# Optimization experiments

Hardware: AMD Instinct MI355X
Metric: run time of the kernel (lower is better)

## Reference

```python
import jax, jax.numpy as jnp
import numpy as np

E = 65536
MUL0, MUL1 = 32, 16              # multiplicities of 0e and 1o in irreps_in1/out
FC_IN, FC_HID = 64, 64
WNUMEL = MUL0*MUL0 + MUL1*MUL0 + MUL0*MUL1 + MUL1*MUL1  # 2304
SILU_NORM = 1.6790                # e3nn normalize2mom constant for silu
ISQRT3 = float(1.0 / np.sqrt(3.0))  # w3j entries for l<=1 paths


def setup_inputs() -> dict:
    key = jax.random.key(0)
    k1, k2, k3, k4, k5 = jax.random.split(key, 5)
    return {
        "fea_in1": jax.random.normal(k1, (E, MUL0 + 3 * MUL1), jnp.float32),
        "fea_in2": jax.random.normal(k2, (E, 4), jnp.float32),
        "fea_weight": jax.random.normal(k3, (E, FC_IN), jnp.float32),
        "W1": jax.random.normal(k4, (FC_IN, FC_HID), jnp.float32),
        "W2": jax.random.normal(k5, (FC_HID, WNUMEL), jnp.float32),
    }


def reference(fea_in1, fea_in2, fea_weight, W1, W2):
    # --- e3nn FullyConnectedNet: variance-preserving linear + normalized silu ---
    h = SILU_NORM * jax.nn.silu(fea_weight @ (W1 / np.sqrt(FC_IN)))   # [E, FC_HID]
    w = h @ (W2 / np.sqrt(FC_HID))                                    # [E, WNUMEL]

    # --- split generated per-edge weights into the 4 uvw paths ---
    s0 = MUL0 * MUL0
    s1 = s0 + MUL1 * MUL0
    s2 = s1 + MUL0 * MUL1
    w00 = w[:, :s0].reshape(E, MUL0, MUL0)     # 0e x 0e -> 0e
    w110 = w[:, s0:s1].reshape(E, MUL1, MUL0)  # 1o x 1o -> 0e
    w011 = w[:, s1:s2].reshape(E, MUL0, MUL1)  # 0e x 1o -> 1o
    w101 = w[:, s2:].reshape(E, MUL1, MUL1)    # 1o x 0e -> 1o

    # --- split irrep blocks ---
    x1_0 = fea_in1[:, :MUL0]                       # [E, 32]
    x1_1 = fea_in1[:, MUL0:].reshape(E, MUL1, 3)   # [E, 16, 3]
    x2_0 = fea_in2[:, 0]                           # [E]
    x2_1 = fea_in2[:, 1:4]                         # [E, 3]

    # path weights: sqrt(ir_out.dim / (mul_in1*mul_in2 * n_paths_to_output))
    pw00 = float(np.sqrt(1.0 / (MUL0 * 2)))
    pw110 = float(np.sqrt(1.0 / (MUL1 * 2)))
    pw011 = float(np.sqrt(3.0 / (MUL0 * 2)))
    pw101 = float(np.sqrt(3.0 / (MUL1 * 2)))

    # CG contractions (w3j(0,0,0)=1, w3j(1,1,0)=delta/sqrt3, w3j(0,1,1)=w3j(1,0,1)=delta/sqrt3)
    out0 = pw00 * jnp.einsum('eu,e,euw->ew', x1_0, x2_0, w00) \
         + (pw110 * ISQRT3) * jnp.einsum('eui,ei,euw->ew', x1_1, x2_1, w110)   # [E, 32]
    out1 = (pw011 * ISQRT3) * jnp.einsum('eu,ek,euw->ewk', x1_0, x2_1, w011) \
         + (pw101 * ISQRT3) * jnp.einsum('eui,e,euw->ewi', x1_1, x2_0, w101)   # [E, 16, 3]

    return jnp.concatenate([out0, out1.reshape(E, 3 * MUL1)], axis=1)          # [E, 80]
```

## Files before the change

### kernel.cpp

```cpp
#include <hip/hip_runtime.h>
#include <hip/hip_bf16.h>

typedef __attribute__((ext_vector_type(8)))  __bf16 bf16x8;
typedef __attribute__((ext_vector_type(16))) float  f32x16;

#define N_TILES   72
#define W2F_ELEMS (72*4*64*8)
#define W1F_ELEMS (2*4*64*8)

__device__ __forceinline__ void gload_lds16(const void* g, void* l) {
    __builtin_amdgcn_global_load_lds(
        (const __attribute__((address_space(1))) unsigned int*)g,
        (__attribute__((address_space(3))) unsigned int*)l, 16, 0, 0);
}

__device__ __forceinline__ unsigned pk_bf16(float a, float b) {
    unsigned r;
    asm("v_cvt_pk_bf16_f32 %0, %1, %2" : "=v"(r) : "v"(a), "v"(b));
    return r;
}

__global__ __launch_bounds__(256) void equiconv_prep(const float* __restrict__ W1,
                                                     const float* __restrict__ W2,
                                                     __bf16* __restrict__ W1F,
                                                     __bf16* __restrict__ W2F) {
    int idx = blockIdx.x * 256 + threadIdx.x;
    if (idx < W2F_ELEMS) {
        int j  = idx & 7;
        int ln = (idx >> 3) & 63;
        int ks = (idx >> 9) & 3;
        int t  = idx >> 11;
        int m  = 32 * t + (ln & 31);
        int c  = ks * 16 + 8 * (ln >> 5) + j;
        W2F[idx] = (__bf16)(W2[c * 2304 + m] * 0.125f);
    } else {
        int i2 = idx - W2F_ELEMS;
        if (i2 < W1F_ELEMS) {
            int j  = i2 & 7;
            int ln = (i2 >> 3) & 63;
            int ks = (i2 >> 9) & 3;
            int mt = i2 >> 11;
            int c  = 32 * mt + (ln & 31);
            int in = ks * 16 + 8 * (ln >> 5) + j;
            W1F[i2] = (__bf16)(W1[in * 64 + c] * 0.125f);
        }
    }
}

#define X10f(u, el)    smemf[(u)*129 + (el)]
#define CB1f(u, el)    smemf[4128 + (u)*129 + (el)]
#define X11f(k, u, el) smemf[6192 + ((u)*3 + (k))*129 + (el)]
#define F2f(el, j)     smemf[12384 + (el)*4 + (j)]
#define ASTG_BASE 12896

__global__ __launch_bounds__(256) void equiconv_main(const float* __restrict__ fea_in1,
                                                     const float* __restrict__ fea_in2,
                                                     const float* __restrict__ fea_w,
                                                     const __bf16* __restrict__ W2F,
                                                     const __bf16* __restrict__ W1F,
                                                     float* __restrict__ out) {
    __shared__ __align__(16) float smemf[14944];

    const int tid  = threadIdx.x;
    const int lane = tid & 63;
    const int wv   = tid >> 6;
    const int l31  = lane & 31;
    const int hi   = lane >> 5;
    const int eBlk = blockIdx.x * 128;
    const int eLoc = wv * 32 + l31;

    for (int i = tid; i < 128 * 80; i += 256) {
        float v = fea_in1[(size_t)eBlk * 80 + i];
        int el = i / 80;
        int j  = i - el * 80;
        if (j < 32) {
            X10f(j, el) = v;
        } else {
            int jj = j - 32;
            int u  = jj / 3;
            int k  = jj - u * 3;
            X11f(k, u, el) = v;
        }
    }
    for (int i = tid; i < 128 * 4; i += 256)
        F2f(i >> 2, i & 3) = fea_in2[(size_t)eBlk * 4 + i];
    __syncthreads();

    const float c110 = 0.10206207261596577f;
    for (int i = tid; i < 16 * 128; i += 256) {
        int u = i >> 7, el = i & 127;
        CB1f(u, el) = c110 * (X11f(0, u, el) * F2f(el, 1) +
                              X11f(1, u, el) * F2f(el, 2) +
                              X11f(2, u, el) * F2f(el, 3));
    }

    const f32x16 Z16 = {0,0,0,0,0,0,0,0,0,0,0,0,0,0,0,0};
    bf16x8 hfr0, hfr1, hfr2, hfr3;
    {
        bf16x8 bw[4];
        const float* pw = fea_w + (size_t)(eBlk + eLoc) * 64 + hi * 8;
#pragma unroll
        for (int ks = 0; ks < 4; ++ks) {
            float4 u0 = *(const float4*)(pw + ks * 16);
            float4 u1 = *(const float4*)(pw + ks * 16 + 4);
            bf16x8 b;
            b[0] = (__bf16)u0.x; b[1] = (__bf16)u0.y; b[2] = (__bf16)u0.z; b[3] = (__bf16)u0.w;
            b[4] = (__bf16)u1.x; b[5] = (__bf16)u1.y; b[6] = (__bf16)u1.z; b[7] = (__bf16)u1.w;
            bw[ks] = b;
        }
        f32x16 h0 = Z16, h1 = Z16;
#pragma unroll
        for (int ks = 0; ks < 4; ++ks) {
            bf16x8 a0 = *(const bf16x8*)(W1F + (size_t)((0 * 4 + ks) * 64 + lane) * 8);
            h0 = __builtin_amdgcn_mfma_f32_32x32x16_bf16(a0, bw[ks], h0, 0, 0, 0);
            bf16x8 a1 = *(const bf16x8*)(W1F + (size_t)((1 * 4 + ks) * 64 + lane) * 8);
            h1 = __builtin_amdgcn_mfma_f32_32x32x16_bf16(a1, bw[ks], h1, 0, 0, 0);
        }
        float sv[32];
#pragma unroll
        for (int r = 0; r < 16; ++r) {
            float x0 = h0[r];
            sv[r]      = 1.679f * x0 / (1.f + __expf(-x0));
            float x1 = h1[r];
            sv[16 + r] = 1.679f * x1 / (1.f + __expf(-x1));
        }
        uint4 fr[4];
#pragma unroll
        for (int ks = 0; ks < 4; ++ks) {
            const int vb = 8 * ks;
            float oa = hi ? sv[vb + 4] : sv[vb + 0];
            float ob = hi ? sv[vb + 5] : sv[vb + 1];
            float oc = hi ? sv[vb + 6] : sv[vb + 2];
            float od = hi ? sv[vb + 7] : sv[vb + 3];
            float sa = hi ? sv[vb + 0] : sv[vb + 4];
            float sb = hi ? sv[vb + 1] : sv[vb + 5];
            float sc = hi ? sv[vb + 2] : sv[vb + 6];
            float sd = hi ? sv[vb + 3] : sv[vb + 7];
            unsigned o0 = pk_bf16(oa, ob), o1 = pk_bf16(oc, od);
            unsigned s0 = pk_bf16(sa, sb), s1 = pk_bf16(sc, sd);
            unsigned r0 = (unsigned)__shfl_xor((int)s0, 32, 64);
            unsigned r1 = (unsigned)__shfl_xor((int)s1, 32, 64);
            fr[ks].x = hi ? r0 : o0;
            fr[ks].y = hi ? r1 : o1;
            fr[ks].z = hi ? o0 : r0;
            fr[ks].w = hi ? o1 : r1;
        }
        hfr0 = *(bf16x8*)&fr[0];
        hfr1 = *(bf16x8*)&fr[1];
        hfr2 = *(bf16x8*)&fr[2];
        hfr3 = *(bf16x8*)&fr[3];
    }

    const float x20  = F2f(eLoc, 0);
    const float x21a = F2f(eLoc, 1), x21b = F2f(eLoc, 2), x21c = F2f(eLoc, 3);
    const float sA0  = 0.125f * x20;
    const float s101 = 0.17677669529663687f * x20;

    float acc0[16];
    float t011[8];
    float t101[3][8];
#pragma unroll
    for (int r = 0; r < 16; ++r) acc0[r] = 0.f;
#pragma unroll
    for (int s = 0; s < 8; ++s) { t011[s] = 0.f; t101[0][s] = 0.f; t101[1][s] = 0.f; t101[2][s] = 0.f; }

    const __bf16* ASTG = (const __bf16*)(smemf + ASTG_BASE);
    char* stgb = (char*)(smemf + ASTG_BASE);
    const char* w2b = (const char*)W2F;

#define STAGE(T, BUF) {                                                           \
        const char* _s = w2b + ((size_t)(T) << 12) + wv * 1024 + (lane << 4);     \
        char* _d = stgb + ((BUF) << 12) + wv * 1024;                              \
        gload_lds16(_s, _d); }

#define EPI_W00(TT) { float cf = sA0 * X10f((TT), eLoc);                          \
        _Pragma("unroll") for (int r = 0; r < 16; ++r) acc0[r] += cf * Cv[r]; }
#define EPI_W110(TT) { float cf = CB1f((TT) - 32, eLoc);                          \
        _Pragma("unroll") for (int r = 0; r < 16; ++r) acc0[r] += cf * Cv[r]; }
#define EPI_W011(TT) { int uu = 2 * ((TT) - 48);                                  \
        float cf0 = X10f(uu, eLoc), cf1 = X10f(uu + 1, eLoc);                     \
        _Pragma("unroll") for (int r = 0; r < 16; ++r)                            \
            t011[r & 7] += (r >= 8 ? cf1 : cf0) * Cv[r]; }
#define EPI_W101(TT) { int uu = 2 * ((TT) - 64);                                  \
        float d00 = X11f(0, uu, eLoc), d01 = X11f(1, uu, eLoc), d02 = X11f(2, uu, eLoc);          \
        float d10 = X11f(0, uu + 1, eLoc), d11 = X11f(1, uu + 1, eLoc), d12 = X11f(2, uu + 1, eLoc); \
        _Pragma("unroll") for (int r = 0; r < 16; ++r) { int s = r & 7;           \
            t101[0][s] += (r >= 8 ? d10 : d00) * Cv[r];                           \
            t101[1][s] += (r >= 8 ? d11 : d01) * Cv[r];                           \
            t101[2][s] += (r >= 8 ? d12 : d02) * Cv[r]; } }

#define TILE_STEP(T, EPI) {                                                       \
        if ((T) + 1 < N_TILES) STAGE((T) + 1, bufx ^ 1);                          \
        const __bf16* tb = ASTG + (bufx << 11) + (lane << 3);                     \
        bf16x8 a0 = *(const bf16x8*)(tb);                                         \
        bf16x8 a1 = *(const bf16x8*)(tb + 512);                                   \
        bf16x8 a2 = *(const bf16x8*)(tb + 1024);                                  \
        bf16x8 a3 = *(const bf16x8*)(tb + 1536);                                  \
        f32x16 Cv;                                                                \
        Cv = __builtin_amdgcn_mfma_f32_32x32x16_bf16(a0, hfr0, Z16, 0, 0, 0);     \
        Cv = __builtin_amdgcn_mfma_f32_32x32x16_bf16(a1, hfr1, Cv, 0, 0, 0);      \
        Cv = __builtin_amdgcn_mfma_f32_32x32x16_bf16(a2, hfr2, Cv, 0, 0, 0);      \
        Cv = __builtin_amdgcn_mfma_f32_32x32x16_bf16(a3, hfr3, Cv, 0, 0, 0);      \
        EPI(T);                                                                   \
        __syncthreads();                                                          \
        bufx ^= 1; }

    int bufx = 0;
    STAGE(0, 0);
    __syncthreads();

#pragma unroll 2
    for (int t = 0; t < 32; ++t) TILE_STEP(t, EPI_W00)
#pragma unroll 2
    for (int t = 32; t < 48; ++t) TILE_STEP(t, EPI_W110)
#pragma unroll 2
    for (int t = 48; t < 64; ++t) TILE_STEP(t, EPI_W011)
#pragma unroll 2
    for (int t = 64; t < 72; ++t) TILE_STEP(t, EPI_W101)

    float* OST = smemf;
#pragma unroll
    for (int r = 0; r < 16; ++r) {
        int rv = (r & 3) + 8 * (r >> 2) + 4 * hi;
        OST[eLoc * 81 + rv] = acc0[r];
    }
#pragma unroll
    for (int s = 0; s < 8; ++s) {
        int w = (s & 3) + 8 * (s >> 2) + 4 * hi;
        float b011 = 0.125f * t011[s];
        OST[eLoc * 81 + 32 + w * 3 + 0] = x21a * b011 + s101 * t101[0][s];
        OST[eLoc * 81 + 32 + w * 3 + 1] = x21b * b011 + s101 * t101[1][s];
        OST[eLoc * 81 + 32 + w * 3 + 2] = x21c * b011 + s101 * t101[2][s];
    }
    __syncthreads();
    {
        float* og = out + (size_t)blockIdx.x * 10240;
        for (int i = tid; i < 10240; i += 256) {
            int el = i / 80;
            int j  = i - el * 80;
            og[i] = OST[el * 81 + j];
        }
    }
}

extern "C" void kernel_launch(void* const* d_in, const int* in_sizes, int n_in,
                              void* d_out, int out_size, void* d_ws, size_t ws_size,
                              hipStream_t stream) {
    const float* fea_in1 = (const float*)d_in[0];
    const float* fea_in2 = (const float*)d_in[1];
    const float* fea_w   = (const float*)d_in[2];
    const float* W1      = (const float*)d_in[3];
    const float* W2      = (const float*)d_in[4];
    __bf16* W2F = (__bf16*)d_ws;
    __bf16* W1F = (__bf16*)((char*)d_ws + (size_t)W2F_ELEMS * 2);

    equiconv_prep<<<(W2F_ELEMS + W1F_ELEMS + 255) / 256, 256, 0, stream>>>(W1, W2, W1F, W2F);
    equiconv_main<<<65536 / 128, 256, 0, stream>>>(fea_in1, fea_in2, fea_w, W2F, W1F, (float*)d_out);
}
```

Measured before the change: 123.8 us.

## Replace double-buffered W2 staging with 8-slot LDS ring and register-resident inputs

Moves per-edge input features (x10, x11, fea_in2, and the cb1 coefficients) out of shared memory into registers. W2 tiles are now staged through an 8-slot LDS ring with 6 tiles prefetched ahead, two tiles per barrier, and explicit vmcnt waits. This replaces a __syncthreads per tile, which halves the barriers and deepens the prefetch. Shared memory shrinks and launch_bounds asks for 2 blocks per CU, but roughly 100 extra live floats per thread risk register pressure or spills.

```diff
diff --git a/kernel.cpp b/kernel.cpp
--- a/kernel.cpp
+++ b/kernel.cpp
@@ -47,19 +47,16 @@
     }
 }
 
-#define X10f(u, el)    smemf[(u)*129 + (el)]
-#define CB1f(u, el)    smemf[4128 + (u)*129 + (el)]
-#define X11f(k, u, el) smemf[6192 + ((u)*3 + (k))*129 + (el)]
-#define F2f(el, j)     smemf[12384 + (el)*4 + (j)]
-#define ASTG_BASE 12896
-
-__global__ __launch_bounds__(256) void equiconv_main(const float* __restrict__ fea_in1,
-                                                     const float* __restrict__ fea_in2,
-                                                     const float* __restrict__ fea_w,
-                                                     const __bf16* __restrict__ W2F,
-                                                     const __bf16* __restrict__ W1F,
-                                                     float* __restrict__ out) {
-    __shared__ __align__(16) float smemf[14944];
+__global__ __launch_bounds__(256, 2) void equiconv_main(const float* __restrict__ fea_in1,
+                                                        const float* __restrict__ fea_in2,
+                                                        const float* __restrict__ fea_w,
+                                                        const __bf16* __restrict__ W2F,
+                                                        const __bf16* __restrict__ W1F,
+                                                        float* __restrict__ out) {
+    __shared__ __align__(16) float smemf[10368];
+    __bf16* RING = (__bf16*)smemf;
+    char*   rgb  = (char*)smemf;
+    const char* w2b = (const char*)W2F;
 
     const int tid  = threadIdx.x;
     const int lane = tid & 63;
@@ -69,30 +66,33 @@
     const int eBlk = blockIdx.x * 128;
     const int eLoc = wv * 32 + l31;
 
-    for (int i = tid; i < 128 * 80; i += 256) {
-        float v = fea_in1[(size_t)eBlk * 80 + i];
-        int el = i / 80;
-        int j  = i - el * 80;
-        if (j < 32) {
-            X10f(j, el) = v;
-        } else {
-            int jj = j - 32;
-            int u  = jj / 3;
-            int k  = jj - u * 3;
-            X11f(k, u, el) = v;
-        }
-    }
-    for (int i = tid; i < 128 * 4; i += 256)
-        F2f(i >> 2, i & 3) = fea_in2[(size_t)eBlk * 4 + i];
-    __syncthreads();
+#define STAGE(T) {                                                                \
+        const char* _s = w2b + ((size_t)(T) << 12) + wv * 1024 + (lane << 4);     \
+        char* _d = rgb + (((T) & 7) << 12) + wv * 1024;                           \
+        gload_lds16(_s, _d); }
+
+    STAGE(0); STAGE(1); STAGE(2); STAGE(3); STAGE(4); STAGE(5);
+
+    const float* r1 = fea_in1 + (size_t)(eBlk + eLoc) * 80;
+    float x10[32];
+#pragma unroll
+    for (int q = 0; q < 8; ++q) {
+        float4 v = *(const float4*)(r1 + 4 * q);
+        x10[4 * q] = v.x; x10[4 * q + 1] = v.y; x10[4 * q + 2] = v.z; x10[4 * q + 3] = v.w;
+    }
+    float x11[48];
+#pragma unroll
+    for (int q = 0; q < 12; ++q) {
+        float4 v = *(const float4*)(r1 + 32 + 4 * q);
+        x11[4 * q] = v.x; x11[4 * q + 1] = v.y; x11[4 * q + 2] = v.z; x11[4 * q + 3] = v.w;
+    }
+    const float4 f2v = *(const float4*)(fea_in2 + (size_t)(eBlk + eLoc) * 4);
 
     const float c110 = 0.10206207261596577f;
-    for (int i = tid; i < 16 * 128; i += 256) {
-        int u = i >> 7, el = i & 127;
-        CB1f(u, el) = c110 * (X11f(0, u, el) * F2f(el, 1) +
-                              X11f(1, u, el) * F2f(el, 2) +
-                              X11f(2, u, el) * F2f(el, 3));
-    }
+    float cb1[16];
+#pragma unroll
+    for (int u = 0; u < 16; ++u)
+        cb1[u] = c110 * (x11[3 * u] * f2v.y + x11[3 * u + 1] * f2v.z + x11[3 * u + 2] * f2v.w);
 
     const f32x16 Z16 = {0,0,0,0,0,0,0,0,0,0,0,0,0,0,0,0};
     bf16x8 hfr0, hfr1, hfr2, hfr3;
@@ -151,11 +151,8 @@
         hfr3 = *(bf16x8*)&fr[3];
     }
 
-    const float x20  = F2f(eLoc, 0);
-    const float x21a = F2f(eLoc, 1), x21b = F2f(eLoc, 2), x21c = F2f(eLoc, 3);
-    const float sA0  = 0.125f * x20;
-    const float s101 = 0.17677669529663687f * x20;
-
+    const float sA0  = 0.125f * f2v.x;
+    const float s101 = 0.17677669529663687f * f2v.x;
     float acc0[16];
     float t011[8];
     float t101[3][8];
@@ -164,34 +161,34 @@
 #pragma unroll
     for (int s = 0; s < 8; ++s) { t011[s] = 0.f; t101[0][s] = 0.f; t101[1][s] = 0.f; t101[2][s] = 0.f; }
 
-    const __bf16* ASTG = (const __bf16*)(smemf + ASTG_BASE);
-    char* stgb = (char*)(smemf + ASTG_BASE);
-    const char* w2b = (const char*)W2F;
-
-#define STAGE(T, BUF) {                                                           \
-        const char* _s = w2b + ((size_t)(T) << 12) + wv * 1024 + (lane << 4);     \
-        char* _d = stgb + ((BUF) << 12) + wv * 1024;                              \
-        gload_lds16(_s, _d); }
-
-#define EPI_W00(TT) { float cf = sA0 * X10f((TT), eLoc);                          \
+#define WAITV4 asm volatile("s_waitcnt vmcnt(4)" ::: "memory")
+#define WAITV2 asm volatile("s_waitcnt vmcnt(2)" ::: "memory")
+#define WAITV0 asm volatile("s_waitcnt vmcnt(0)" ::: "memory")
+
+#define EPI_W00(TT) { float cf = sA0 * x10[(TT)];                                 \
         _Pragma("unroll") for (int r = 0; r < 16; ++r) acc0[r] += cf * Cv[r]; }
-#define EPI_W110(TT) { float cf = CB1f((TT) - 32, eLoc);                          \
+#define EPI_W110(TT) { float cf = cb1[(TT) - 32];                                 \
         _Pragma("unroll") for (int r = 0; r < 16; ++r) acc0[r] += cf * Cv[r]; }
-#define EPI_W011(TT) { int uu = 2 * ((TT) - 48);                                  \
-        float cf0 = X10f(uu, eLoc), cf1 = X10f(uu + 1, eLoc);                     \
+#define EPI_W011(TT) { const int uu = 2 * ((TT) - 48);                            \
+        float cf0 = x10[uu], cf1 = x10[uu + 1];                                   \
         _Pragma("unroll") for (int r = 0; r < 16; ++r)                            \
             t011[r & 7] += (r >= 8 ? cf1 : cf0) * Cv[r]; }
-#define EPI_W101(TT) { int uu = 2 * ((TT) - 64);                                  \
-        float d00 = X11f(0, uu, eLoc), d01 = X11f(1, uu, eLoc), d02 = X11f(2, uu, eLoc);          \
-        float d10 = X11f(0, uu + 1, eLoc), d11 = X11f(1, uu + 1, eLoc), d12 = X11f(2, uu + 1, eLoc); \
+#define EPI_W101(TT) { const int uu = 2 * ((TT) - 64);                            \
+        float d00 = x11[3*uu+0],   d01 = x11[3*uu+1],   d02 = x11[3*uu+2];        \
+        float d10 = x11[3*uu+3],   d11 = x11[3*uu+4],   d12 = x11[3*uu+5];        \
         _Pragma("unroll") for (int r = 0; r < 16; ++r) { int s = r & 7;           \
             t101[0][s] += (r >= 8 ? d10 : d00) * Cv[r];                           \
             t101[1][s] += (r >= 8 ? d11 : d01) * Cv[r];                           \
             t101[2][s] += (r >= 8 ? d12 : d02) * Cv[r]; } }
 
-#define TILE_STEP(T, EPI) {                                                       \
-        if ((T) + 1 < N_TILES) STAGE((T) + 1, bufx ^ 1);                          \
-        const __bf16* tb = ASTG + (bufx << 11) + (lane << 3);                     \
+#define EPI_ANY(TT) {                                                             \
+        if ((TT) < 32)      { EPI_W00(TT) }                                       \
+        else if ((TT) < 48) { EPI_W110(TT) }                                      \
+        else if ((TT) < 64) { EPI_W011(TT) }                                      \
+        else                { EPI_W101(TT) } }
+
+#define DO_TILE(TT) {                                                             \
+        const __bf16* tb = RING + (((TT) & 7) << 11) + (lane << 3);               \
         bf16x8 a0 = *(const bf16x8*)(tb);                                         \
         bf16x8 a1 = *(const bf16x8*)(tb + 512);                                   \
         bf16x8 a2 = *(const bf16x8*)(tb + 1024);                                  \
@@ -201,23 +198,23 @@
         Cv = __builtin_amdgcn_mfma_f32_32x32x16_bf16(a1, hfr1, Cv, 0, 0, 0);      \
         Cv = __builtin_amdgcn_mfma_f32_32x32x16_bf16(a2, hfr2, Cv, 0, 0, 0);      \
         Cv = __builtin_amdgcn_mfma_f32_32x32x16_bf16(a3, hfr3, Cv, 0, 0, 0);      \
-        EPI(T);                                                                   \
-        __syncthreads();                                                          \
-        bufx ^= 1; }
-
-    int bufx = 0;
-    STAGE(0, 0);
+        EPI_ANY(TT); }
+
+    WAITV0;
+
+#pragma unroll
+    for (int i = 0; i < 36; ++i) {
+        if (i < 34)       { WAITV4; }
+        else if (i == 34) { WAITV2; }
+        else              { WAITV0; }
+        __builtin_amdgcn_s_barrier();
+        __builtin_amdgcn_sched_barrier(0);
+        if (2 * i + 6 < N_TILES) { STAGE(2 * i + 6); STAGE(2 * i + 7); }
+        DO_TILE(2 * i);
+        DO_TILE(2 * i + 1);
+    }
+
     __syncthreads();
-
-#pragma unroll 2
-    for (int t = 0; t < 32; ++t) TILE_STEP(t, EPI_W00)
-#pragma unroll 2
-    for (int t = 32; t < 48; ++t) TILE_STEP(t, EPI_W110)
-#pragma unroll 2
-    for (int t = 48; t < 64; ++t) TILE_STEP(t, EPI_W011)
-#pragma unroll 2
-    for (int t = 64; t < 72; ++t) TILE_STEP(t, EPI_W101)
-
     float* OST = smemf;
 #pragma unroll
     for (int r = 0; r < 16; ++r) {
@@ -228,9 +225,9 @@
     for (int s = 0; s < 8; ++s) {
         int w = (s & 3) + 8 * (s >> 2) + 4 * hi;
         float b011 = 0.125f * t011[s];
-        OST[eLoc * 81 + 32 + w * 3 + 0] = x21a * b011 + s101 * t101[0][s];
-        OST[eLoc * 81 + 32 + w * 3 + 1] = x21b * b011 + s101 * t101[1][s];
-        OST[eLoc * 81 + 32 + w * 3 + 2] = x21c * b011 + s101 * t101[2][s];
+        OST[eLoc * 81 + 32 + w * 3 + 0] = f2v.y * b011 + s101 * t101[0][s];
+        OST[eLoc * 81 + 32 + w * 3 + 1] = f2v.z * b011 + s101 * t101[1][s];
+        OST[eLoc * 81 + 32 + w * 3 + 2] = f2v.w * b011 + s101 * t101[2][s];
     }
     __syncthreads();
     {
```

Measured after the change: 112.2 us. 9.4% less time.
